# Optimization experiments

Measured on AMD Instinct MI355X. Metric: run time of the kernel, lower is better.

The kernel has to match this reference:

```python
import jax, jax.numpy as jnp
import numpy as np

N_NODES = 100000
N_EDGES = 1600000
FEAT, HID, OUT = 256, 128, 64
N_BATCH = 10000
EPS = 1e-5


def gcn_conv(x, src, dst, W, b, n):
    # PyG GCNConv: linear -> add self loops -> sym-normalized scatter-add -> bias
    h = x @ W  # [N, C]
    loop = jnp.arange(n, dtype=src.dtype)
    s = jnp.concatenate([src, loop])
    d = jnp.concatenate([dst, loop])
    deg = jax.ops.segment_sum(jnp.ones_like(d, dtype=h.dtype), d, num_segments=n)
    dinv = jnp.where(deg > 0, jax.lax.rsqrt(deg), 0.0)
    norm = dinv[s] * dinv[d]                    # [E+N]
    msg = h[s] * norm[:, None]                  # gather + scale
    out = jax.ops.segment_sum(msg, d, num_segments=n)  # scatter-add
    return out + b


def batch_norm(x, gamma, beta):
    # training-mode BatchNorm1d: batch statistics, biased variance
    mu = jnp.mean(x, axis=0)
    var = jnp.var(x, axis=0)
    return (x - mu) * jax.lax.rsqrt(var + EPS) * gamma + beta


def setup_inputs() -> dict:
    key = jax.random.key(0)
    ks = jax.random.split(key, 8)
    features = jax.random.normal(ks[0], (N_NODES, FEAT), dtype=jnp.float32)
    edge_index = jax.random.randint(ks[1], (2, N_EDGES), 0, N_NODES, dtype=jnp.int64 if jax.config.jax_enable_x64 else jnp.int32)
    batch_nodes = jax.random.randint(ks[2], (N_BATCH,), 0, N_NODES, dtype=jnp.int32)
    W1 = jax.random.normal(ks[3], (FEAT, HID), dtype=jnp.float32) * (1.0 / np.sqrt(FEAT))
    b1 = jnp.zeros((HID,), jnp.float32)
    gamma1 = jnp.ones((HID,), jnp.float32)
    beta1 = jnp.zeros((HID,), jnp.float32)
    W2 = jax.random.normal(ks[4], (HID, OUT), dtype=jnp.float32) * (1.0 / np.sqrt(HID))
    b2 = jnp.zeros((OUT,), jnp.float32)
    gamma2 = jnp.ones((OUT,), jnp.float32)
    beta2 = jnp.zeros((OUT,), jnp.float32)
    return {"features": features, "edge_index": edge_index, "batch_nodes": batch_nodes,
            "W1": W1, "b1": b1, "gamma1": gamma1, "beta1": beta1,
            "W2": W2, "b2": b2, "gamma2": gamma2, "beta2": beta2}


def reference(features, edge_index, batch_nodes, W1, b1, gamma1, beta1, W2, b2, gamma2, beta2):
    src, dst = edge_index[0], edge_index[1]
    n = features.shape[0]
    x = gcn_conv(features, src, dst, W1, b1, n)
    x = jax.nn.relu(batch_norm(x, gamma1, beta1))
    # dropout treated as identity (deterministic reference)
    x = gcn_conv(x, src, dst, W2, b2, n)
    x = jax.nn.relu(batch_norm(x, gamma2, beta2))
    return jax.nn.log_softmax(x[batch_nodes], axis=1)
```

## Files before the change

kernel.cpp:

```cpp
#include <hip/hip_runtime.h>
#include <stdint.h>

typedef unsigned short bf16_t;

constexpr int kNN   = 100000;
constexpr int kNE   = 1600000;
constexpr int kFEAT = 256;
constexpr int kHID  = 128;
constexpr int kOUT  = 64;
constexpr int kNB   = 10000;
constexpr float kEPS = 1e-5f;

constexpr int kEPB  = 4096;
constexpr int kNBLK = (kNE + kEPB - 1) / kEPB;
constexpr int kNBUK = (kNN + 511) / 512;

typedef __attribute__((ext_vector_type(8))) short short8v;
typedef __attribute__((ext_vector_type(4))) float f32x4;

__device__ __forceinline__ float bf2f(bf16_t u) {
    union { uint32_t i; float f; } v; v.i = ((uint32_t)u) << 16; return v.f;
}
__device__ __forceinline__ bf16_t f2bf(float f) {
    uint32_t u = __float_as_uint(f);
    uint32_t r = (u + 0x7FFFu + ((u >> 16) & 1u)) >> 16;
    return (bf16_t)r;
}
__device__ __forceinline__ float lo16(uint32_t u) {
    union { uint32_t i; float f; } v; v.i = u << 16; return v.f;
}
__device__ __forceinline__ float hi16(uint32_t u) {
    union { uint32_t i; float f; } v; v.i = u & 0xFFFF0000u; return v.f;
}

__global__ void k_probe(const uint32_t* __restrict__ feat, const uint32_t* __restrict__ ei,
                        int* __restrict__ flags) {
    int l = threadIdx.x;
    int good = 0;
    for (int j = l; j < 256; j += 64) {
        uint32_t e = (feat[j] >> 7) & 0xFFu;
        if (e >= 100u && e <= 132u) good++;
    }
    for (int o = 32; o; o >>= 1) good += __shfl_xor(good, o);
    int zeros = 0;
    for (int j = l; j < 128; j += 64) zeros += (ei[2 * j + 1] == 0u) ? 1 : 0;
    for (int o = 32; o; o >>= 1) zeros += __shfl_xor(zeros, o);
    if (l == 0) {
        flags[0] = (good > 128) ? 1 : 0;
        flags[1] = (zeros > 64) ? 1 : 0;
    }
}


__global__ void k_hist1(const int* __restrict__ ei, const int* __restrict__ flags,
                        unsigned int* __restrict__ counts) {
    __shared__ unsigned int lh[kNBUK];
    int t = threadIdx.x;
    for (int i = t; i < kNBUK; i += 256) lh[i] = 0u;
    __syncthreads();
    int i64 = flags[1];
    int base = blockIdx.x * kEPB;
    for (int k = 0; k < 16; k++) {
        int e = base + k * 256 + t;
        if (e < kNE) {
            int d = i64 ? ei[2 * (kNE + e)] : ei[kNE + e];
            atomicAdd(&lh[d >> 9], 1u);
        }
    }
    __syncthreads();
    for (int i = t; i < kNBUK; i += 256) counts[(size_t)i * kNBLK + blockIdx.x] = lh[i];
}

__global__ void k_scanA(const unsigned int* __restrict__ counts, unsigned int* __restrict__ base,
                        float* __restrict__ stats) {
    __shared__ unsigned int ss[256];
    int t = threadIdx.x;
    for (int i = t; i < 384; i += 256) stats[i] = 0.f;
    unsigned int tot = 0u;
    if (t < kNBUK) {
        const unsigned int* row = counts + (size_t)t * kNBLK;
        for (int j = 0; j < kNBLK; j++) tot += row[j];
    }
    ss[t] = tot;
    __syncthreads();
    for (int o = 1; o < 256; o <<= 1) {
        unsigned int x = (t >= o) ? ss[t - o] : 0u;
        __syncthreads();
        ss[t] += x;
        __syncthreads();
    }
    if (t < kNBUK) base[t] = ss[t] - tot;
    if (t == 0) base[kNBUK] = ss[255];
}

__global__ void k_scanB(const unsigned int* __restrict__ counts, const unsigned int* __restrict__ base,
                        unsigned int* __restrict__ off) {
    __shared__ unsigned int ss[64];
    int b = blockIdx.x, t = threadIdx.x;
    unsigned int run = base[b];
    for (int c0 = 0; c0 < kNBLK; c0 += 64) {
        int idx = c0 + t;
        unsigned int v = (idx < kNBLK) ? counts[(size_t)b * kNBLK + idx] : 0u;
        ss[t] = v;
        __syncthreads();
        for (int o = 1; o < 64; o <<= 1) {
            unsigned int x = (t >= o) ? ss[t - o] : 0u;
            __syncthreads();
            ss[t] += x;
            __syncthreads();
        }
        if (idx < kNBLK) off[(size_t)b * kNBLK + idx] = run + ss[t] - v;
        unsigned int ctot = ss[63];
        __syncthreads();
        run += ctot;
    }
}

__global__ void k_scatter1(const int* __restrict__ ei, const int* __restrict__ flags,
                           const unsigned int* __restrict__ off, unsigned int* __restrict__ pairs) {
    __shared__ unsigned int lcur[kNBUK];
    int t = threadIdx.x;
    for (int i = t; i < kNBUK; i += 256) lcur[i] = off[(size_t)i * kNBLK + blockIdx.x];
    __syncthreads();
    int i64 = flags[1];
    int base = blockIdx.x * kEPB;
    for (int k = 0; k < 16; k++) {
        int e = base + k * 256 + t;
        if (e < kNE) {
            int s, d;
            if (i64) { s = ei[2 * e]; d = ei[2 * (kNE + e)]; }
            else     { s = ei[e];     d = ei[kNE + e]; }
            unsigned int p = atomicAdd(&lcur[d >> 9], 1u);
            pairs[p] = (unsigned int)s | ((unsigned int)(d & 511) << 17);
        }
    }
}

__global__ void __launch_bounds__(1024) k_scatter2(const unsigned int* __restrict__ pairs,
                        const unsigned int* __restrict__ base, unsigned int* __restrict__ deg,
                        float* __restrict__ dinv, unsigned int* __restrict__ cursor,
                        int* __restrict__ sorted) {
    __shared__ unsigned int hist[512], sc[512], lcur[512];
    int b = blockIdx.x, t = threadIdx.x;
    unsigned int gb = base[b];
    int cnt = (int)(base[b + 1] - gb);
    if (t < 512) hist[t] = 0u;
    __syncthreads();
    for (int i = t; i < cnt; i += 1024) atomicAdd(&hist[pairs[gb + i] >> 17], 1u);
    __syncthreads();
    if (t < 512) sc[t] = hist[t];
    __syncthreads();
    for (int o = 1; o < 512; o <<= 1) {
        unsigned int x = 0u;
        if (t < 512 && t >= o) x = sc[t - o];
        __syncthreads();
        if (t < 512) sc[t] += x;
        __syncthreads();
    }
    if (t < 512) {
        lcur[t] = gb + sc[t] - hist[t];
        int node = b * 512 + t;
        if (node < kNN) {
            unsigned int dg = hist[t] + 1u;
            deg[node] = dg;
            dinv[node] = rsqrtf((float)dg);
            cursor[node] = gb + sc[t];
        }
    }
    __syncthreads();
    for (int i = t; i < cnt; i += 1024) {
        unsigned int pk = pairs[gb + i];
        unsigned int slot = atomicAdd(&lcur[pk >> 17], 1u);
        sorted[slot] = (int)(pk & 0x1FFFFu);
    }
}

__global__ void k_prepw(const void* __restrict__ W1, const void* __restrict__ W2,
                        const int* __restrict__ flags, bf16_t* __restrict__ Wz1,
                        bf16_t* __restrict__ Wz2) {
    int gid = blockIdx.x * 256 + threadIdx.x;
    int isbf = flags[0];
    if (gid < 4096) {
        int idx = gid;
        int l = idx & 63, j = (idx >> 6) & 7, t = idx >> 9;
        int col = j * 16 + (l & 15);
        int kb = t * 32 + (l >> 4) * 8;
        bf16_t o[8];
        if (isbf) {
            const bf16_t* Wb = (const bf16_t*)W1;
            #pragma unroll
            for (int i = 0; i < 8; i++) o[i] = Wb[(size_t)(kb + i) * kHID + col];
        } else {
            const float* Wf = (const float*)W1;
            #pragma unroll
            for (int i = 0; i < 8; i++) o[i] = f2bf(Wf[(size_t)(kb + i) * kHID + col]);
        }
        uint4 w;
        w.x = (uint32_t)o[0] | ((uint32_t)o[1] << 16);
        w.y = (uint32_t)o[2] | ((uint32_t)o[3] << 16);
        w.z = (uint32_t)o[4] | ((uint32_t)o[5] << 16);
        w.w = (uint32_t)o[6] | ((uint32_t)o[7] << 16);
        *(uint4*)(Wz1 + (size_t)idx * 8) = w;
    } else if (gid < 4096 + 1024) {
        int idx = gid - 4096;
        int l = idx & 63, j = (idx >> 6) & 3, t = idx >> 8;
        int col = j * 16 + (l & 15);
        int kb = t * 32 + (l >> 4) * 8;
        bf16_t o[8];
        if (isbf) {
            const bf16_t* Wb = (const bf16_t*)W2;
            #pragma unroll
            for (int i = 0; i < 8; i++) o[i] = Wb[(size_t)(kb + i) * kOUT + col];
        } else {
            const float* Wf = (const float*)W2;
            #pragma unroll
            for (int i = 0; i < 8; i++) o[i] = f2bf(Wf[(size_t)(kb + i) * kOUT + col]);
        }
        uint4 w;
        w.x = (uint32_t)o[0] | ((uint32_t)o[1] << 16);
        w.y = (uint32_t)o[2] | ((uint32_t)o[3] << 16);
        w.z = (uint32_t)o[4] | ((uint32_t)o[5] << 16);
        w.w = (uint32_t)o[6] | ((uint32_t)o[7] << 16);
        *(uint4*)(Wz2 + (size_t)idx * 8) = w;
    }
}

__global__ void k_gemm1(const void* __restrict__ A, const bf16_t* __restrict__ Wz,
                        const float* __restrict__ dinv, bf16_t* __restrict__ H,
                        const int* __restrict__ flags) {
    int isbf = flags[0];
    int wv = threadIdx.x >> 6;
    int l  = threadIdx.x & 63;
    int kgrp = l >> 4;
    int rbase = blockIdx.x * 128 + wv * 32;
    int arow0 = rbase + (l & 15);
    int arow1 = arow0 + 16;
    const bf16_t* Ab = (const bf16_t*)A;
    const float*  Af = (const float*)A;
    const short8v* Wv = (const short8v*)Wz;

    f32x4 acc[2][8];
    #pragma unroll
    for (int m = 0; m < 2; m++)
        #pragma unroll
        for (int j = 0; j < 8; j++)
            acc[m][j] = (f32x4){0.f, 0.f, 0.f, 0.f};

    #pragma unroll
    for (int t = 0; t < 8; t++) {
        int kbase = t * 32 + kgrp * 8;
        short8v a0, a1;
        #pragma unroll
        for (int i = 0; i < 8; i++) { a0[i] = 0; a1[i] = 0; }
        if (arow0 < kNN) {
            if (isbf) {
                a0 = *(const short8v*)(Ab + (size_t)arow0 * kFEAT + kbase);
            } else {
                const float* p = Af + (size_t)arow0 * kFEAT + kbase;
                #pragma unroll
                for (int i = 0; i < 8; i++) a0[i] = (short)f2bf(p[i]);
            }
        }
        if (arow1 < kNN) {
            if (isbf) {
                a1 = *(const short8v*)(Ab + (size_t)arow1 * kFEAT + kbase);
            } else {
                const float* p = Af + (size_t)arow1 * kFEAT + kbase;
                #pragma unroll
                for (int i = 0; i < 8; i++) a1[i] = (short)f2bf(p[i]);
            }
        }
        #pragma unroll
        for (int j = 0; j < 8; j++) {
            short8v b = Wv[(t * 8 + j) * 64 + l];
            acc[0][j] = __builtin_amdgcn_mfma_f32_16x16x32_bf16(a0, b, acc[0][j], 0, 0, 0);
            acc[1][j] = __builtin_amdgcn_mfma_f32_16x16x32_bf16(a1, b, acc[1][j], 0, 0, 0);
        }
    }

    #pragma unroll
    for (int m = 0; m < 2; m++) {
        #pragma unroll
        for (int r = 0; r < 4; r++) {
            int orow = rbase + m * 16 + kgrp * 4 + r;
            if (orow < kNN) {
                float dn = dinv[orow];
                bf16_t* hp = H + (size_t)orow * kHID + (l & 15);
                #pragma unroll
                for (int j = 0; j < 8; j++) hp[j * 16] = f2bf(acc[m][j][r] * dn);
            }
        }
    }
}

__global__ void k_agg1(const bf16_t* __restrict__ H, const int* __restrict__ sorted,
                       const unsigned int* __restrict__ cursor, const unsigned int* __restrict__ deg,
                       const float* __restrict__ dinv, const void* __restrict__ bias,
                       const int* __restrict__ flags, float* __restrict__ Out,
                       float* __restrict__ stats) {
    __shared__ float ss[256];
    int t = threadIdx.x;
    ss[t] = 0.f;
    int wv = t >> 6;
    int lane = t & 63;
    int c0 = lane * 2;
    float b0, b1v;
    if (flags[0]) { b0 = bf2f(((const bf16_t*)bias)[c0]); b1v = bf2f(((const bf16_t*)bias)[c0 + 1]); }
    else          { b0 = ((const float*)bias)[c0];        b1v = ((const float*)bias)[c0 + 1]; }
    const uint32_t* Hrow = (const uint32_t*)H;
    float ps0 = 0.f, ps1 = 0.f, pq0 = 0.f, pq1 = 0.f;
    for (int n = blockIdx.x * 4 + wv; n < kNN; n += gridDim.x * 4) {
        float dn = dinv[n];
        uint32_t hu = Hrow[(size_t)n * 64 + lane];
        float acc0 = lo16(hu), acc1 = hi16(hu);
        unsigned int e1 = cursor[n];
        int cnt = (int)(deg[n] - 1u);
        unsigned int e = e1 - (unsigned int)cnt;
        for (; cnt >= 8; cnt -= 8, e += 8) {
            int s0 = sorted[e],     s1 = sorted[e + 1], s2 = sorted[e + 2], s3 = sorted[e + 3];
            int s4 = sorted[e + 4], s5 = sorted[e + 5], s6 = sorted[e + 6], s7 = sorted[e + 7];
            uint32_t u0 = Hrow[(size_t)s0 * 64 + lane];
            uint32_t u1 = Hrow[(size_t)s1 * 64 + lane];
            uint32_t u2 = Hrow[(size_t)s2 * 64 + lane];
            uint32_t u3 = Hrow[(size_t)s3 * 64 + lane];
            uint32_t u4 = Hrow[(size_t)s4 * 64 + lane];
            uint32_t u5 = Hrow[(size_t)s5 * 64 + lane];
            uint32_t u6 = Hrow[(size_t)s6 * 64 + lane];
            uint32_t u7 = Hrow[(size_t)s7 * 64 + lane];
            acc0 += lo16(u0) + lo16(u1) + lo16(u2) + lo16(u3)
                  + lo16(u4) + lo16(u5) + lo16(u6) + lo16(u7);
            acc1 += hi16(u0) + hi16(u1) + hi16(u2) + hi16(u3)
                  + hi16(u4) + hi16(u5) + hi16(u6) + hi16(u7);
        }
        for (; cnt > 0; cnt--, e++) {
            uint32_t u = Hrow[(size_t)sorted[e] * 64 + lane];
            acc0 += lo16(u);
            acc1 += hi16(u);
        }
        float ox = acc0 * dn + b0;
        float oy = acc1 * dn + b1v;
        float2 o; o.x = ox; o.y = oy;
        *(float2*)(Out + (size_t)n * kHID + c0) = o;
        ps0 += ox; ps1 += oy; pq0 += ox * ox; pq1 += oy * oy;
    }
    __syncthreads();
    atomicAdd(&ss[c0], ps0);
    atomicAdd(&ss[c0 + 1], ps1);
    atomicAdd(&ss[128 + c0], pq0);
    atomicAdd(&ss[128 + c0 + 1], pq1);
    __syncthreads();
    atomicAdd(&stats[t], ss[t]);
}

__global__ void k_bnprep(const float* __restrict__ stats, const void* __restrict__ gamma,
                         const void* __restrict__ beta, const int* __restrict__ flags,
                         float* __restrict__ bnp) {
    int c = threadIdx.x;
    float mu = stats[c] * (1.f / kNN);
    float var = stats[128 + c] * (1.f / kNN) - mu * mu;
    float rs = rsqrtf(var + kEPS);
    float g, b;
    if (flags[0]) { g = bf2f(((const bf16_t*)gamma)[c]); b = bf2f(((const bf16_t*)beta)[c]); }
    else          { g = ((const float*)gamma)[c];        b = ((const float*)beta)[c]; }
    float sc = rs * g;
    bnp[c] = sc;
    bnp[128 + c] = b - mu * sc;
}

__global__ void k_gemm2(const float* A, const bf16_t* __restrict__ Wz,
                        const float* __restrict__ dinv, const float* __restrict__ bnp,
                        bf16_t* H ) {
    int wv = threadIdx.x >> 6;
    int l  = threadIdx.x & 63;
    int kgrp = l >> 4;
    int rbase = blockIdx.x * 128 + wv * 32;
    int arow0 = rbase + (l & 15);
    int arow1 = arow0 + 16;
    const short8v* Wv = (const short8v*)Wz;

    f32x4 acc[2][4];
    #pragma unroll
    for (int m = 0; m < 2; m++)
        #pragma unroll
        for (int j = 0; j < 4; j++)
            acc[m][j] = (f32x4){0.f, 0.f, 0.f, 0.f};

    #pragma unroll
    for (int t = 0; t < 4; t++) {
        int kbase = t * 32 + kgrp * 8;
        float4 sa = *(const float4*)(bnp + kbase);
        float4 sb = *(const float4*)(bnp + kbase + 4);
        float4 ha = *(const float4*)(bnp + 128 + kbase);
        float4 hb = *(const float4*)(bnp + 128 + kbase + 4);
        short8v a0, a1;
        #pragma unroll
        for (int i = 0; i < 8; i++) { a0[i] = 0; a1[i] = 0; }
        if (arow0 < kNN) {
            float4 f0 = *(const float4*)(A + (size_t)arow0 * kHID + kbase);
            float4 f1 = *(const float4*)(A + (size_t)arow0 * kHID + kbase + 4);
            float v;
            v = f0.x * sa.x + ha.x; a0[0] = (short)f2bf(v > 0.f ? v : 0.f);
            v = f0.y * sa.y + ha.y; a0[1] = (short)f2bf(v > 0.f ? v : 0.f);
            v = f0.z * sa.z + ha.z; a0[2] = (short)f2bf(v > 0.f ? v : 0.f);
            v = f0.w * sa.w + ha.w; a0[3] = (short)f2bf(v > 0.f ? v : 0.f);
            v = f1.x * sb.x + hb.x; a0[4] = (short)f2bf(v > 0.f ? v : 0.f);
            v = f1.y * sb.y + hb.y; a0[5] = (short)f2bf(v > 0.f ? v : 0.f);
            v = f1.z * sb.z + hb.z; a0[6] = (short)f2bf(v > 0.f ? v : 0.f);
            v = f1.w * sb.w + hb.w; a0[7] = (short)f2bf(v > 0.f ? v : 0.f);
        }
        if (arow1 < kNN) {
            float4 f0 = *(const float4*)(A + (size_t)arow1 * kHID + kbase);
            float4 f1 = *(const float4*)(A + (size_t)arow1 * kHID + kbase + 4);
            float v;
            v = f0.x * sa.x + ha.x; a1[0] = (short)f2bf(v > 0.f ? v : 0.f);
            v = f0.y * sa.y + ha.y; a1[1] = (short)f2bf(v > 0.f ? v : 0.f);
            v = f0.z * sa.z + ha.z; a1[2] = (short)f2bf(v > 0.f ? v : 0.f);
            v = f0.w * sa.w + ha.w; a1[3] = (short)f2bf(v > 0.f ? v : 0.f);
            v = f1.x * sb.x + hb.x; a1[4] = (short)f2bf(v > 0.f ? v : 0.f);
            v = f1.y * sb.y + hb.y; a1[5] = (short)f2bf(v > 0.f ? v : 0.f);
            v = f1.z * sb.z + hb.z; a1[6] = (short)f2bf(v > 0.f ? v : 0.f);
            v = f1.w * sb.w + hb.w; a1[7] = (short)f2bf(v > 0.f ? v : 0.f);
        }
        #pragma unroll
        for (int j = 0; j < 4; j++) {
            short8v b = Wv[(t * 4 + j) * 64 + l];
            acc[0][j] = __builtin_amdgcn_mfma_f32_16x16x32_bf16(a0, b, acc[0][j], 0, 0, 0);
            acc[1][j] = __builtin_amdgcn_mfma_f32_16x16x32_bf16(a1, b, acc[1][j], 0, 0, 0);
        }
    }

    #pragma unroll
    for (int m = 0; m < 2; m++) {
        #pragma unroll
        for (int r = 0; r < 4; r++) {
            int orow = rbase + m * 16 + kgrp * 4 + r;
            if (orow < kNN) {
                float dn = dinv[orow];
                bf16_t* hp = H + (size_t)orow * 256 + (l & 15);
                #pragma unroll
                for (int j = 0; j < 4; j++) hp[j * 16] = f2bf(acc[m][j][r] * dn);
            }
        }
    }
}

__global__ void k_agg2(const bf16_t* __restrict__ H, const int* __restrict__ sorted,
                       const unsigned int* __restrict__ cursor, const unsigned int* __restrict__ deg,
                       const float* __restrict__ dinv, const void* __restrict__ bias,
                       const int* __restrict__ flags, float* __restrict__ Out,
                       float* __restrict__ stats) {
    __shared__ float ss[128];
    int t = threadIdx.x;
    if (t < 128) ss[t] = 0.f;
    int grp = t >> 5;
    int lane = t & 31;
    int c0 = lane * 2;
    float b0, b1v;
    if (flags[0]) { b0 = bf2f(((const bf16_t*)bias)[c0]); b1v = bf2f(((const bf16_t*)bias)[c0 + 1]); }
    else          { b0 = ((const float*)bias)[c0];        b1v = ((const float*)bias)[c0 + 1]; }
    const uint32_t* Hrow = (const uint32_t*)H;
    float ps0 = 0.f, ps1 = 0.f, pq0 = 0.f, pq1 = 0.f;
    for (int n = blockIdx.x * 8 + grp; n < kNN; n += gridDim.x * 8) {
        float dn = dinv[n];
        uint32_t hu = Hrow[(size_t)n * 128 + lane];
        float acc0 = lo16(hu), acc1 = hi16(hu);
        unsigned int e1 = cursor[n];
        int cnt = (int)(deg[n] - 1u);
        unsigned int e = e1 - (unsigned int)cnt;
        for (; cnt >= 8; cnt -= 8, e += 8) {
            int s0 = sorted[e],     s1 = sorted[e + 1], s2 = sorted[e + 2], s3 = sorted[e + 3];
            int s4 = sorted[e + 4], s5 = sorted[e + 5], s6 = sorted[e + 6], s7 = sorted[e + 7];
            uint32_t u0 = Hrow[(size_t)s0 * 128 + lane];
            uint32_t u1 = Hrow[(size_t)s1 * 128 + lane];
            uint32_t u2 = Hrow[(size_t)s2 * 128 + lane];
            uint32_t u3 = Hrow[(size_t)s3 * 128 + lane];
            uint32_t u4 = Hrow[(size_t)s4 * 128 + lane];
            uint32_t u5 = Hrow[(size_t)s5 * 128 + lane];
            uint32_t u6 = Hrow[(size_t)s6 * 128 + lane];
            uint32_t u7 = Hrow[(size_t)s7 * 128 + lane];
            acc0 += lo16(u0) + lo16(u1) + lo16(u2) + lo16(u3)
                  + lo16(u4) + lo16(u5) + lo16(u6) + lo16(u7);
            acc1 += hi16(u0) + hi16(u1) + hi16(u2) + hi16(u3)
                  + hi16(u4) + hi16(u5) + hi16(u6) + hi16(u7);
        }
        for (; cnt > 0; cnt--, e++) {
            uint32_t u = Hrow[(size_t)sorted[e] * 128 + lane];
            acc0 += lo16(u);
            acc1 += hi16(u);
        }
        float ox = acc0 * dn + b0;
        float oy = acc1 * dn + b1v;
        float2 o; o.x = ox; o.y = oy;
        *(float2*)(Out + (size_t)n * kOUT + c0) = o;
        ps0 += ox; ps1 += oy; pq0 += ox * ox; pq1 += oy * oy;
    }
    __syncthreads();
    atomicAdd(&ss[c0], ps0);
    atomicAdd(&ss[c0 + 1], ps1);
    atomicAdd(&ss[64 + c0], pq0);
    atomicAdd(&ss[64 + c0 + 1], pq1);
    __syncthreads();
    if (t < 64)  atomicAdd(&stats[256 + t], ss[t]);
    else if (t < 128) atomicAdd(&stats[320 + (t - 64)], ss[t]);
}

__global__ void k_out(const float* __restrict__ A2, const float* __restrict__ stats,
                      const int* __restrict__ batch, const void* __restrict__ gamma,
                      const void* __restrict__ beta, const int* __restrict__ flags,
                      bf16_t* __restrict__ out) {
    int wid = threadIdx.x >> 6;
    int lane = threadIdx.x & 63;
    int i = blockIdx.x * 4 + wid;
    if (i >= kNB) return;
    int n = batch[i];
    int c = lane;
    float mu = stats[256 + c] * (1.f / kNN);
    float var = stats[320 + c] * (1.f / kNN) - mu * mu;
    float g, b;
    if (flags[0]) { g = bf2f(((const bf16_t*)gamma)[c]); b = bf2f(((const bf16_t*)beta)[c]); }
    else          { g = ((const float*)gamma)[c];        b = ((const float*)beta)[c]; }
    float v = (A2[(size_t)n * kOUT + c] - mu) * rsqrtf(var + kEPS) * g + b;
    v = v > 0.f ? v : 0.f;
    float m = v;
    for (int o = 32; o; o >>= 1) m = fmaxf(m, __shfl_xor(m, o));
    float ex = expf(v - m);
    float s = ex;
    for (int o = 32; o; o >>= 1) s += __shfl_xor(s, o);
    float r = v - m - logf(s);
    if (flags[0]) out[(size_t)i * kOUT + c] = f2bf(r);
    else ((float*)out)[(size_t)i * kOUT + c] = r;
}

static inline size_t align_up(size_t x, size_t a) { return (x + a - 1) & ~(a - 1); }

extern "C" void kernel_launch(void* const* d_in, const int* in_sizes, int n_in,
                              void* d_out, int out_size, void* d_ws, size_t ws_size,
                              hipStream_t stream) {
    (void)in_sizes; (void)n_in; (void)out_size; (void)ws_size;
    const void* feat = d_in[0];
    const int* ei    = (const int*)d_in[1];
    const int* batch = (const int*)d_in[2];
    const void* W1   = d_in[3];
    const void* b1   = d_in[4];
    const void* g1   = d_in[5];
    const void* be1  = d_in[6];
    const void* W2   = d_in[7];
    const void* b2   = d_in[8];
    const void* g2   = d_in[9];
    const void* be2  = d_in[10];

    char* ws = (char*)d_ws;
    size_t o = 0;
    int*          flags  = (int*)(ws + o);          o = align_up(o + 32, 256);
    unsigned int* deg    = (unsigned int*)(ws + o); o = align_up(o + (size_t)kNN * 4, 256);
    float*        dinv   = (float*)(ws + o);        o = align_up(o + (size_t)kNN * 4, 256);
    unsigned int* cursor = (unsigned int*)(ws + o); o = align_up(o + (size_t)kNN * 4, 256);
    float*        stats  = (float*)(ws + o);        o = align_up(o + 384 * 4, 256);
    float*        bnp    = (float*)(ws + o);        o = align_up(o + 256 * 4, 256);
    int*          sorted = (int*)(ws + o);          o = align_up(o + (size_t)kNE * 4, 256);
    bf16_t*       h1     = (bf16_t*)(ws + o);       o = align_up(o + (size_t)kNN * kHID * 2, 256);
    float*        a1     = (float*)(ws + o);        o = align_up(o + (size_t)kNN * kHID * 4, 256);
    bf16_t*       wz1    = (bf16_t*)(ws + o);       o = align_up(o + (size_t)8 * 8 * 64 * 8 * 2, 256);
    bf16_t*       wz2    = (bf16_t*)(ws + o);       o = align_up(o + (size_t)4 * 4 * 64 * 8 * 2, 256);

    unsigned int* pairs  = (unsigned int*)h1;
    unsigned int* counts = (unsigned int*)a1;
    unsigned int* offm   = (unsigned int*)((char*)a1 + 512 * 1024);
    unsigned int* gbase  = (unsigned int*)((char*)a1 + 1024 * 1024);

    bf16_t*       h2 = (bf16_t*)a1;
    float*        a2 = (float*)h1;

    bf16_t* outp = (bf16_t*)d_out;

    k_probe   <<<1, 64, 0, stream>>>((const uint32_t*)feat, (const uint32_t*)ei, flags);
    k_prepw   <<<20, 256, 0, stream>>>(W1, W2, flags, wz1, wz2);
    k_hist1   <<<kNBLK, 256, 0, stream>>>(ei, flags, counts);
    k_scanA   <<<1, 256, 0, stream>>>(counts, gbase, stats);
    k_scanB   <<<kNBUK, 64, 0, stream>>>(counts, gbase, offm);
    k_scatter1<<<kNBLK, 256, 0, stream>>>(ei, flags, offm, pairs);
    k_scatter2<<<kNBUK, 1024, 0, stream>>>(pairs, gbase, deg, dinv, cursor, sorted);

    k_gemm1 <<<(kNN + 127) / 128, 256, 0, stream>>>(feat, wz1, dinv, h1, flags);
    k_agg1  <<<2048, 256, 0, stream>>>(h1, sorted, cursor, deg, dinv, b1, flags, a1, stats);
    k_bnprep<<<1, 128, 0, stream>>>(stats, g1, be1, flags, bnp);

    k_gemm2<<<(kNN + 127) / 128, 256, 0, stream>>>(a1, wz2, dinv, bnp, h2);
    k_agg2 <<<1024, 256, 0, stream>>>(h2, sorted, cursor, deg, dinv, b2, flags, a2, stats);

    k_out<<<(kNB + 3) / 4, 256, 0, stream>>>(a2, stats, batch, g2, be2, flags, outp);
}
```

Before: 477.8 us.

## Split BN statistics out of aggregation kernels and launch one node per wavefront

The aggregation kernels now process exactly one destination node per wave or half-wave, with a grid sized to the node count, instead of a grid-stride loop over a fixed grid. The per-column batch-norm sum and sum-of-squares reduction moves into separate k_stat1/k_stat2 kernels that re-read the aggregated output. This drops the shared-memory atomics and tail synchronisation from the latency-bound gather kernels and gives more independent work for load balancing. The cost is two extra launches and an additional full read of the 51 MB and 25 MB activations.

```diff
diff --git a/kernel.cpp b/kernel.cpp
--- a/kernel.cpp
+++ b/kernel.cpp
@@ -296,60 +296,60 @@
 __global__ void k_agg1(const bf16_t* __restrict__ H, const int* __restrict__ sorted,
                        const unsigned int* __restrict__ cursor, const unsigned int* __restrict__ deg,
                        const float* __restrict__ dinv, const void* __restrict__ bias,
-                       const int* __restrict__ flags, float* __restrict__ Out,
-                       float* __restrict__ stats) {
-    __shared__ float ss[256];
+                       const int* __restrict__ flags, float* __restrict__ Out) {
     int t = threadIdx.x;
-    ss[t] = 0.f;
     int wv = t >> 6;
     int lane = t & 63;
     int c0 = lane * 2;
+    int n = blockIdx.x * 4 + wv;
     float b0, b1v;
     if (flags[0]) { b0 = bf2f(((const bf16_t*)bias)[c0]); b1v = bf2f(((const bf16_t*)bias)[c0 + 1]); }
     else          { b0 = ((const float*)bias)[c0];        b1v = ((const float*)bias)[c0 + 1]; }
     const uint32_t* Hrow = (const uint32_t*)H;
-    float ps0 = 0.f, ps1 = 0.f, pq0 = 0.f, pq1 = 0.f;
-    for (int n = blockIdx.x * 4 + wv; n < kNN; n += gridDim.x * 4) {
-        float dn = dinv[n];
-        uint32_t hu = Hrow[(size_t)n * 64 + lane];
-        float acc0 = lo16(hu), acc1 = hi16(hu);
-        unsigned int e1 = cursor[n];
-        int cnt = (int)(deg[n] - 1u);
-        unsigned int e = e1 - (unsigned int)cnt;
-        for (; cnt >= 8; cnt -= 8, e += 8) {
-            int s0 = sorted[e],     s1 = sorted[e + 1], s2 = sorted[e + 2], s3 = sorted[e + 3];
-            int s4 = sorted[e + 4], s5 = sorted[e + 5], s6 = sorted[e + 6], s7 = sorted[e + 7];
-            uint32_t u0 = Hrow[(size_t)s0 * 64 + lane];
-            uint32_t u1 = Hrow[(size_t)s1 * 64 + lane];
-            uint32_t u2 = Hrow[(size_t)s2 * 64 + lane];
-            uint32_t u3 = Hrow[(size_t)s3 * 64 + lane];
-            uint32_t u4 = Hrow[(size_t)s4 * 64 + lane];
-            uint32_t u5 = Hrow[(size_t)s5 * 64 + lane];
-            uint32_t u6 = Hrow[(size_t)s6 * 64 + lane];
-            uint32_t u7 = Hrow[(size_t)s7 * 64 + lane];
-            acc0 += lo16(u0) + lo16(u1) + lo16(u2) + lo16(u3)
-                  + lo16(u4) + lo16(u5) + lo16(u6) + lo16(u7);
-            acc1 += hi16(u0) + hi16(u1) + hi16(u2) + hi16(u3)
-                  + hi16(u4) + hi16(u5) + hi16(u6) + hi16(u7);
-        }
-        for (; cnt > 0; cnt--, e++) {
-            uint32_t u = Hrow[(size_t)sorted[e] * 64 + lane];
-            acc0 += lo16(u);
-            acc1 += hi16(u);
-        }
-        float ox = acc0 * dn + b0;
-        float oy = acc1 * dn + b1v;
-        float2 o; o.x = ox; o.y = oy;
-        *(float2*)(Out + (size_t)n * kHID + c0) = o;
-        ps0 += ox; ps1 += oy; pq0 += ox * ox; pq1 += oy * oy;
-    }
-    __syncthreads();
-    atomicAdd(&ss[c0], ps0);
-    atomicAdd(&ss[c0 + 1], ps1);
-    atomicAdd(&ss[128 + c0], pq0);
-    atomicAdd(&ss[128 + c0 + 1], pq1);
-    __syncthreads();
-    atomicAdd(&stats[t], ss[t]);
+    float dn = dinv[n];
+    uint32_t hu = Hrow[(size_t)n * 64 + lane];
+    float acc0 = lo16(hu), acc1 = hi16(hu);
+    unsigned int e1 = cursor[n];
+    int cnt = (int)(deg[n] - 1u);
+    unsigned int e = e1 - (unsigned int)cnt;
+    for (; cnt >= 8; cnt -= 8, e += 8) {
+        int s0 = sorted[e],     s1 = sorted[e + 1], s2 = sorted[e + 2], s3 = sorted[e + 3];
+        int s4 = sorted[e + 4], s5 = sorted[e + 5], s6 = sorted[e + 6], s7 = sorted[e + 7];
+        uint32_t u0 = Hrow[(size_t)s0 * 64 + lane];
+        uint32_t u1 = Hrow[(size_t)s1 * 64 + lane];
+        uint32_t u2 = Hrow[(size_t)s2 * 64 + lane];
+        uint32_t u3 = Hrow[(size_t)s3 * 64 + lane];
+        uint32_t u4 = Hrow[(size_t)s4 * 64 + lane];
+        uint32_t u5 = Hrow[(size_t)s5 * 64 + lane];
+        uint32_t u6 = Hrow[(size_t)s6 * 64 + lane];
+        uint32_t u7 = Hrow[(size_t)s7 * 64 + lane];
+        acc0 += lo16(u0) + lo16(u1) + lo16(u2) + lo16(u3)
+              + lo16(u4) + lo16(u5) + lo16(u6) + lo16(u7);
+        acc1 += hi16(u0) + hi16(u1) + hi16(u2) + hi16(u3)
+              + hi16(u4) + hi16(u5) + hi16(u6) + hi16(u7);
+    }
+    for (; cnt > 0; cnt--, e++) {
+        uint32_t u = Hrow[(size_t)sorted[e] * 64 + lane];
+        acc0 += lo16(u);
+        acc1 += hi16(u);
+    }
+    float2 o; o.x = acc0 * dn + b0; o.y = acc1 * dn + b1v;
+    *(float2*)(Out + (size_t)n * kHID + c0) = o;
+}
+
+__global__ void k_stat1(const float* __restrict__ A1, float* __restrict__ stats) {
+    int c = threadIdx.x & 127;
+    int r0 = threadIdx.x >> 7;
+    int chunk = (kNN + gridDim.x - 1) / gridDim.x;
+    int nbeg = blockIdx.x * chunk;
+    int nend = nbeg + chunk; if (nend > kNN) nend = kNN;
+    float s0 = 0.f, s1 = 0.f;
+    for (int n = nbeg + r0; n < nend; n += 2) {
+        float v = A1[(size_t)n * kHID + c];
+        s0 += v; s1 += v * v;
+    }
+    atomicAdd(&stats[c], s0);
+    atomicAdd(&stats[kHID + c], s1);
 }
 
 __global__ void k_bnprep(const float* __restrict__ stats, const void* __restrict__ gamma,
@@ -447,61 +447,60 @@
 __global__ void k_agg2(const bf16_t* __restrict__ H, const int* __restrict__ sorted,
                        const unsigned int* __restrict__ cursor, const unsigned int* __restrict__ deg,
                        const float* __restrict__ dinv, const void* __restrict__ bias,
-                       const int* __restrict__ flags, float* __restrict__ Out,
-                       float* __restrict__ stats) {
-    __shared__ float ss[128];
+                       const int* __restrict__ flags, float* __restrict__ Out) {
     int t = threadIdx.x;
-    if (t < 128) ss[t] = 0.f;
     int grp = t >> 5;
     int lane = t & 31;
     int c0 = lane * 2;
+    int n = blockIdx.x * 8 + grp;
     float b0, b1v;
     if (flags[0]) { b0 = bf2f(((const bf16_t*)bias)[c0]); b1v = bf2f(((const bf16_t*)bias)[c0 + 1]); }
     else          { b0 = ((const float*)bias)[c0];        b1v = ((const float*)bias)[c0 + 1]; }
     const uint32_t* Hrow = (const uint32_t*)H;
-    float ps0 = 0.f, ps1 = 0.f, pq0 = 0.f, pq1 = 0.f;
-    for (int n = blockIdx.x * 8 + grp; n < kNN; n += gridDim.x * 8) {
-        float dn = dinv[n];
-        uint32_t hu = Hrow[(size_t)n * 128 + lane];
-        float acc0 = lo16(hu), acc1 = hi16(hu);
-        unsigned int e1 = cursor[n];
-        int cnt = (int)(deg[n] - 1u);
-        unsigned int e = e1 - (unsigned int)cnt;
-        for (; cnt >= 8; cnt -= 8, e += 8) {
-            int s0 = sorted[e],     s1 = sorted[e + 1], s2 = sorted[e + 2], s3 = sorted[e + 3];
-            int s4 = sorted[e + 4], s5 = sorted[e + 5], s6 = sorted[e + 6], s7 = sorted[e + 7];
-            uint32_t u0 = Hrow[(size_t)s0 * 128 + lane];
-            uint32_t u1 = Hrow[(size_t)s1 * 128 + lane];
-            uint32_t u2 = Hrow[(size_t)s2 * 128 + lane];
-            uint32_t u3 = Hrow[(size_t)s3 * 128 + lane];
-            uint32_t u4 = Hrow[(size_t)s4 * 128 + lane];
-            uint32_t u5 = Hrow[(size_t)s5 * 128 + lane];
-            uint32_t u6 = Hrow[(size_t)s6 * 128 + lane];
-            uint32_t u7 = Hrow[(size_t)s7 * 128 + lane];
-            acc0 += lo16(u0) + lo16(u1) + lo16(u2) + lo16(u3)
-                  + lo16(u4) + lo16(u5) + lo16(u6) + lo16(u7);
-            acc1 += hi16(u0) + hi16(u1) + hi16(u2) + hi16(u3)
-                  + hi16(u4) + hi16(u5) + hi16(u6) + hi16(u7);
-        }
-        for (; cnt > 0; cnt--, e++) {
-            uint32_t u = Hrow[(size_t)sorted[e] * 128 + lane];
-            acc0 += lo16(u);
-            acc1 += hi16(u);
-        }
-        float ox = acc0 * dn + b0;
-        float oy = acc1 * dn + b1v;
-        float2 o; o.x = ox; o.y = oy;
-        *(float2*)(Out + (size_t)n * kOUT + c0) = o;
-        ps0 += ox; ps1 += oy; pq0 += ox * ox; pq1 += oy * oy;
-    }
-    __syncthreads();
-    atomicAdd(&ss[c0], ps0);
-    atomicAdd(&ss[c0 + 1], ps1);
-    atomicAdd(&ss[64 + c0], pq0);
-    atomicAdd(&ss[64 + c0 + 1], pq1);
-    __syncthreads();
-    if (t < 64)  atomicAdd(&stats[256 + t], ss[t]);
-    else if (t < 128) atomicAdd(&stats[320 + (t - 64)], ss[t]);
+    float dn = dinv[n];
+    uint32_t hu = Hrow[(size_t)n * 128 + lane];
+    float acc0 = lo16(hu), acc1 = hi16(hu);
+    unsigned int e1 = cursor[n];
+    int cnt = (int)(deg[n] - 1u);
+    unsigned int e = e1 - (unsigned int)cnt;
+    for (; cnt >= 8; cnt -= 8, e += 8) {
+        int s0 = sorted[e],     s1 = sorted[e + 1], s2 = sorted[e + 2], s3 = sorted[e + 3];
+        int s4 = sorted[e + 4], s5 = sorted[e + 5], s6 = sorted[e + 6], s7 = sorted[e + 7];
+        uint32_t u0 = Hrow[(size_t)s0 * 128 + lane];
+        uint32_t u1 = Hrow[(size_t)s1 * 128 + lane];
+        uint32_t u2 = Hrow[(size_t)s2 * 128 + lane];
+        uint32_t u3 = Hrow[(size_t)s3 * 128 + lane];
+        uint32_t u4 = Hrow[(size_t)s4 * 128 + lane];
+        uint32_t u5 = Hrow[(size_t)s5 * 128 + lane];
+        uint32_t u6 = Hrow[(size_t)s6 * 128 + lane];
+        uint32_t u7 = Hrow[(size_t)s7 * 128 + lane];
+        acc0 += lo16(u0) + lo16(u1) + lo16(u2) + lo16(u3)
+              + lo16(u4) + lo16(u5) + lo16(u6) + lo16(u7);
+        acc1 += hi16(u0) + hi16(u1) + hi16(u2) + hi16(u3)
+              + hi16(u4) + hi16(u5) + hi16(u6) + hi16(u7);
+    }
+    for (; cnt > 0; cnt--, e++) {
+        uint32_t u = Hrow[(size_t)sorted[e] * 128 + lane];
+        acc0 += lo16(u);
+        acc1 += hi16(u);
+    }
+    float2 o; o.x = acc0 * dn + b0; o.y = acc1 * dn + b1v;
+    *(float2*)(Out + (size_t)n * kOUT + c0) = o;
+}
+
+__global__ void k_stat2(const float* __restrict__ A2, float* __restrict__ stats) {
+    int c = threadIdx.x & 63;
+    int r0 = threadIdx.x >> 6;
+    int chunk = (kNN + gridDim.x - 1) / gridDim.x;
+    int nbeg = blockIdx.x * chunk;
+    int nend = nbeg + chunk; if (nend > kNN) nend = kNN;
+    float s0 = 0.f, s1 = 0.f;
+    for (int n = nbeg + r0; n < nend; n += 4) {
+        float v = A2[(size_t)n * kOUT + c];
+        s0 += v; s1 += v * v;
+    }
+    atomicAdd(&stats[256 + c], s0);
+    atomicAdd(&stats[320 + c], s1);
 }
 
 __global__ void k_out(const float* __restrict__ A2, const float* __restrict__ stats,
@@ -582,11 +581,13 @@
     k_scatter2<<<kNBUK, 1024, 0, stream>>>(pairs, gbase, deg, dinv, cursor, sorted);
 
     k_gemm1 <<<(kNN + 127) / 128, 256, 0, stream>>>(feat, wz1, dinv, h1, flags);
-    k_agg1  <<<2048, 256, 0, stream>>>(h1, sorted, cursor, deg, dinv, b1, flags, a1, stats);
+    k_agg1  <<<kNN / 4, 256, 0, stream>>>(h1, sorted, cursor, deg, dinv, b1, flags, a1);
+    k_stat1 <<<256, 256, 0, stream>>>(a1, stats);
     k_bnprep<<<1, 128, 0, stream>>>(stats, g1, be1, flags, bnp);
 
     k_gemm2<<<(kNN + 127) / 128, 256, 0, stream>>>(a1, wz2, dinv, bnp, h2);
-    k_agg2 <<<1024, 256, 0, stream>>>(h2, sorted, cursor, deg, dinv, b2, flags, a2, stats);
+    k_agg2 <<<kNN / 8, 256, 0, stream>>>(h2, sorted, cursor, deg, dinv, b2, flags, a2);
+    k_stat2<<<256, 256, 0, stream>>>(a2, stats);
 
     k_out<<<(kNB + 3) / 4, 256, 0, stream>>>(a2, stats, batch, g2, be2, flags, outp);
 }
```

Measured after the change: 501.8 us. +5.0%, slower.
